# Kernel optimization log

Hardware: AMD Instinct MI355X
Metric: run time of the kernel (lower is better)

The kernel has to match this reference:

```python
import jax, jax.numpy as jnp
import numpy as np

N_NODES = 100000
N_EDGES = 1600000
NUM_FEATURES = 128
NUM_CLASSES = 10
NUM_GRAPHS = 64


def setup_inputs() -> dict:
    key = jax.random.key(0)
    ks = jax.random.split(key, 16)
    x = jax.random.normal(ks[0], (N_NODES, NUM_FEATURES), dtype=jnp.float32)
    edge_index = jax.random.randint(ks[1], (2, N_EDGES), 0, N_NODES, dtype=jnp.int64)
    batch = jnp.sort(jax.random.randint(ks[2], (N_NODES,), 0, NUM_GRAPHS, dtype=jnp.int64))

    def glorot(k, fan_in, fan_out):
        s = jnp.sqrt(6.0 / (fan_in + fan_out)).astype(jnp.float32)
        return jax.random.uniform(k, (fan_in, fan_out), jnp.float32, -s, s)

    dims = [(NUM_FEATURES, 128), (128, 128), (128, 128), (128, 64), (64, 32)]
    params = {}
    for i, (fi, fo) in enumerate(dims, start=1):
        params[f"W{i}"] = glorot(ks[2 + i], fi, fo)
        params[f"b{i}"] = jnp.zeros((fo,), jnp.float32)
    params["Wfc"] = glorot(ks[10], 32, NUM_CLASSES)
    params["bfc"] = jnp.zeros((NUM_CLASSES,), jnp.float32)
    return {"x": x, "edge_index": edge_index, "batch": batch, **params}


def reference(x, edge_index, batch, W1, b1, W2, b2, W3, b3, W4, b4, W5, b5, Wfc, bfc):
    N = x.shape[0]
    loops = jnp.arange(N, dtype=edge_index.dtype)
    src = jnp.concatenate([edge_index[0], loops])  # message source j
    dst = jnp.concatenate([edge_index[1], loops])  # message target i
    # GCN symmetric normalization: deg computed on targets incl. self loops
    deg = jax.ops.segment_sum(jnp.ones_like(dst, x.dtype), dst, num_segments=N)
    dinv = jnp.where(deg > 0, jax.lax.rsqrt(deg), 0.0)
    norm = (dinv[src] * dinv[dst])[:, None]  # [E+N, 1]

    def gcn_conv(h, W, b):
        h = h @ W  # transform first (smaller gather width when out < in)
        msg = h[src] * norm
        return jax.ops.segment_sum(msg, dst, num_segments=N) + b

    h = jax.nn.relu(gcn_conv(x, W1, b1))
    h = jax.nn.relu(gcn_conv(h, W2, b2))
    h = jax.nn.relu(gcn_conv(h, W3, b3))
    h = jax.nn.relu(gcn_conv(h, W4, b4))
    h = jax.nn.relu(gcn_conv(h, W5, b5))

    # global_mean_pool over graph membership
    sums = jax.ops.segment_sum(h, batch, num_segments=NUM_GRAPHS)
    cnts = jax.ops.segment_sum(jnp.ones((N,), h.dtype), batch, num_segments=NUM_GRAPHS)
    pooled = sums / jnp.maximum(cnts, 1.0)[:, None]

    # dropout is identity in eval mode
    return pooled @ Wfc + bfc
```

## Files before the change

kernel.cpp:

```cpp
#include <hip/hip_runtime.h>
#include <hip/hip_bf16.h>

#define N_NODES 100000
#define N_EDGES 1600000
#define N_GRAPHS 64
#define WNB 192
#define BCAP 64

typedef __attribute__((ext_vector_type(8))) short bf16x8;
typedef __attribute__((ext_vector_type(4))) float f32x4;

__device__ inline float bflo(unsigned u) { return __uint_as_float(u << 16); }
__device__ inline float bfhi(unsigned u) { return __uint_as_float(u & 0xffff0000u); }
__device__ inline unsigned short f2bf(float f) {
    unsigned u = __float_as_uint(f);
    return (unsigned short)((u + 0x7fff + ((u >> 16) & 1)) >> 16);
}


__global__ __launch_bounds__(256) void k_setup(int* __restrict__ cursor, int n,
                                               const float* __restrict__ W1,
                                               const float* __restrict__ W2,
                                               const float* __restrict__ W3,
                                               const float* __restrict__ W4,
                                               const float* __restrict__ W5,
                                               unsigned short* __restrict__ wt1,
                                               unsigned short* __restrict__ wt2,
                                               unsigned short* __restrict__ wt3,
                                               unsigned short* __restrict__ wt4,
                                               unsigned short* __restrict__ wt5) {
    const int nb = (N_NODES + 255) / 256;
    if ((int)blockIdx.x < nb) {
        int i = blockIdx.x * 256 + threadIdx.x;
        if (i < n) cursor[i] = i * BCAP;
        return;
    }
    int i = (blockIdx.x - nb) * 256 + threadIdx.x;
    const float* W; unsigned short* WT; int FI, FO, j;
    if (i < 16384)      { W = W1; WT = wt1; FI = 128; FO = 128; j = i; }
    else if (i < 32768) { W = W2; WT = wt2; FI = 128; FO = 128; j = i - 16384; }
    else if (i < 49152) { W = W3; WT = wt3; FI = 128; FO = 128; j = i - 32768; }
    else if (i < 57344) { W = W4; WT = wt4; FI = 128; FO = 64;  j = i - 49152; }
    else if (i < 59392) { W = W5; WT = wt5; FI = 64;  FO = 32;  j = i - 57344; }
    else return;
    int n_ = j / FI, k_ = j % FI;
    WT[j] = f2bf(W[(size_t)k_ * FO + n_]);
}


__global__ __launch_bounds__(256) void k_fillw(const int* __restrict__ ei,
                                               int* __restrict__ cursor,
                                               int* __restrict__ cols, int e) {
    const int w = blockIdx.x & 7;
    const int b = blockIdx.x >> 3;
    const int lo = w * 12500, hi = lo + 12500;
    const int4* d4 = (const int4*)(ei + e);
    const int n4 = e >> 2;
    for (int i = b * 256 + threadIdx.x; i < n4; i += WNB * 256) {
        int4 d = d4[i];
        int base = 4 * i;
        if (d.x >= lo && d.x < hi) {
            int p = atomicAdd(&cursor[d.x], 1);
            if (p < d.x * BCAP + BCAP) cols[p] = ei[base];
        }
        if (d.y >= lo && d.y < hi) {
            int p = atomicAdd(&cursor[d.y], 1);
            if (p < d.y * BCAP + BCAP) cols[p] = ei[base + 1];
        }
        if (d.z >= lo && d.z < hi) {
            int p = atomicAdd(&cursor[d.z], 1);
            if (p < d.z * BCAP + BCAP) cols[p] = ei[base + 2];
        }
        if (d.w >= lo && d.w < hi) {
            int p = atomicAdd(&cursor[d.w], 1);
            if (p < d.w * BCAP + BCAP) cols[p] = ei[base + 3];
        }
    }
}


template <int FI, int FO>
__global__ __launch_bounds__(256) void k_gemm1(const float* __restrict__ Ain,
                                               const unsigned short* __restrict__ WT,
                                               unsigned short* __restrict__ Tout,
                                               const int* __restrict__ cursor,
                                               float* __restrict__ dinv, int n) {
    {
        int gi = blockIdx.x * 256 + threadIdx.x;
        if (gi < n) dinv[gi] = rsqrtf((float)(cursor[gi] - BCAP * gi + 1));
    }
    constexpr int NT = FO / 16;
    constexpr int NC = FI / 32;
    __shared__ unsigned short tile[4][16][FO];
    const int wave = threadIdx.x >> 6;
    const int lane = threadIdx.x & 63;
    const int m = lane & 15;
    const int q = lane >> 4;
    const int row0 = blockIdx.x * 64 + wave * 16;
    int arow = row0 + m;
    if (arow > n - 1) arow = n - 1;

    f32x4 acc[NT];
    #pragma unroll
    for (int j = 0; j < NT; j++) acc[j] = (f32x4){0.f, 0.f, 0.f, 0.f};

    #pragma unroll
    for (int c = 0; c < NC; c++) {
        const int k0 = c * 32 + q * 8;
        const float* ap = Ain + (size_t)arow * FI + k0;
        float4 f0 = *reinterpret_cast<const float4*>(ap);
        float4 f1 = *reinterpret_cast<const float4*>(ap + 4);
        bf16x8 a;
        a[0] = (short)f2bf(f0.x); a[1] = (short)f2bf(f0.y);
        a[2] = (short)f2bf(f0.z); a[3] = (short)f2bf(f0.w);
        a[4] = (short)f2bf(f1.x); a[5] = (short)f2bf(f1.y);
        a[6] = (short)f2bf(f1.z); a[7] = (short)f2bf(f1.w);
        #pragma unroll
        for (int j = 0; j < NT; j++) {
            bf16x8 b = *reinterpret_cast<const bf16x8*>(
                           WT + (size_t)(j * 16 + m) * FI + k0);
            acc[j] = __builtin_amdgcn_mfma_f32_16x16x32_bf16(a, b, acc[j], 0, 0, 0);
        }
    }

    #pragma unroll
    for (int r = 0; r < 4; r++)
        #pragma unroll
        for (int j = 0; j < NT; j++)
            tile[wave][q * 4 + r][j * 16 + m] = f2bf(acc[j][r]);

    constexpr int CPR = FO / 8;
    constexpr int ITERS = 16 * CPR / 64;
    #pragma unroll
    for (int it = 0; it < ITERS; it++) {
        int idx = it * 64 + lane;
        int rr = idx / CPR;
        int cc = idx % CPR;
        int row = row0 + rr;
        if (row < n) {
            uint4 v = *reinterpret_cast<const uint4*>(&tile[wave][rr][cc * 8]);
            *reinterpret_cast<uint4*>(&Tout[(size_t)row * FO + cc * 8]) = v;
        }
    }
}


template <int FA, int FB, int UNR>
__global__ __launch_bounds__(256) void k_fused(const unsigned short* __restrict__ T,
                                               const int* __restrict__ cursor,
                                               const int* __restrict__ cols,
                                               const float* __restrict__ dinv,
                                               const float* __restrict__ bias,
                                               const unsigned short* __restrict__ WT,
                                               unsigned short* __restrict__ Tout, int n) {
    constexpr int LPE = FA / 8;
    constexpr int EPW = 64 / LPE;
    constexpr int STR = FA + 8;
    __shared__ unsigned short hrow[16][STR];

    const int w = threadIdx.x >> 6;
    const int lane = threadIdx.x & 63;
    const int sub = lane / LPE;
    const int li  = lane % LPE;
    const int node0 = blockIdx.x * 16;

    for (int i = 0; i < 4; i++) {
        const int r = w * 4 + i;
        int node = node0 + r;
        bool valid = node < n;
        if (node > n - 1) node = n - 1;
        node = __builtin_amdgcn_readfirstlane(node);

        const float dn = dinv[node];
        float acc[8];
        #pragma unroll
        for (int k = 0; k < 8; k++) acc[k] = 0.f;

        if (sub == 0) {
            float dii = dn * dn;
            uint4 u = reinterpret_cast<const uint4*>(T + (size_t)node * FA)[li];
            acc[0] = dii * bflo(u.x); acc[1] = dii * bfhi(u.x);
            acc[2] = dii * bflo(u.y); acc[3] = dii * bfhi(u.y);
            acc[4] = dii * bflo(u.z); acc[5] = dii * bfhi(u.z);
            acc[6] = dii * bflo(u.w); acc[7] = dii * bfhi(u.w);
        }

        const int e0 = node * BCAP;
        int e1 = cursor[node];
        if (e1 > e0 + BCAP) e1 = e0 + BCAP;
        int e = e0 + sub;
        for (; e + (UNR - 1) * EPW < e1; e += UNR * EPW) {
            int cs[UNR]; float ws[UNR]; uint4 tv[UNR];
            #pragma unroll
            for (int u = 0; u < UNR; u++)
                cs[u] = __builtin_nontemporal_load(&cols[e + u * EPW]);
            #pragma unroll
            for (int u = 0; u < UNR; u++)
                tv[u] = reinterpret_cast<const uint4*>(T + (size_t)cs[u] * FA)[li];
            #pragma unroll
            for (int u = 0; u < UNR; u++)
                ws[u] = dinv[cs[u]] * dn;
            #pragma unroll
            for (int u = 0; u < UNR; u++) {
                float wv = ws[u];
                acc[0] += wv * bflo(tv[u].x); acc[1] += wv * bfhi(tv[u].x);
                acc[2] += wv * bflo(tv[u].y); acc[3] += wv * bfhi(tv[u].y);
                acc[4] += wv * bflo(tv[u].z); acc[5] += wv * bfhi(tv[u].z);
                acc[6] += wv * bflo(tv[u].w); acc[7] += wv * bfhi(tv[u].w);
            }
        }
        for (; e < e1; e += EPW) {
            int c = __builtin_nontemporal_load(&cols[e]);
            uint4 tv = reinterpret_cast<const uint4*>(T + (size_t)c * FA)[li];
            float wv = dinv[c] * dn;
            acc[0] += wv * bflo(tv.x); acc[1] += wv * bfhi(tv.x);
            acc[2] += wv * bflo(tv.y); acc[3] += wv * bfhi(tv.y);
            acc[4] += wv * bflo(tv.z); acc[5] += wv * bfhi(tv.z);
            acc[6] += wv * bflo(tv.w); acc[7] += wv * bfhi(tv.w);
        }

        #pragma unroll
        for (int off = LPE; off < 64; off <<= 1) {
            #pragma unroll
            for (int k = 0; k < 8; k++) acc[k] += __shfl_xor(acc[k], off);
        }

        if (sub == 0) {
            uint4 pk = {0u, 0u, 0u, 0u};
            if (valid) {
                float4 ba = reinterpret_cast<const float4*>(bias)[2 * li];
                float4 bb = reinterpret_cast<const float4*>(bias)[2 * li + 1];
                float r0 = fmaxf(acc[0] + ba.x, 0.f);
                float r1 = fmaxf(acc[1] + ba.y, 0.f);
                float r2 = fmaxf(acc[2] + ba.z, 0.f);
                float r3 = fmaxf(acc[3] + ba.w, 0.f);
                float r4 = fmaxf(acc[4] + bb.x, 0.f);
                float r5 = fmaxf(acc[5] + bb.y, 0.f);
                float r6 = fmaxf(acc[6] + bb.z, 0.f);
                float r7 = fmaxf(acc[7] + bb.w, 0.f);
                pk.x = (unsigned)f2bf(r0) | ((unsigned)f2bf(r1) << 16);
                pk.y = (unsigned)f2bf(r2) | ((unsigned)f2bf(r3) << 16);
                pk.z = (unsigned)f2bf(r4) | ((unsigned)f2bf(r5) << 16);
                pk.w = (unsigned)f2bf(r6) | ((unsigned)f2bf(r7) << 16);
            }
            *reinterpret_cast<uint4*>(&hrow[r][li * 8]) = pk;
        }
    }

    __syncthreads();

    constexpr int NTILES = FB / 16;
    constexpr int NC = FA / 32;
    const int m = lane & 15;
    const int q = lane >> 4;

    for (int j = w; j < NTILES; j += 4) {
        f32x4 acc = (f32x4){0.f, 0.f, 0.f, 0.f};
        #pragma unroll
        for (int c = 0; c < NC; c++) {
            const int k0 = c * 32 + q * 8;
            bf16x8 a = *reinterpret_cast<const bf16x8*>(&hrow[m][k0]);
            bf16x8 b = *reinterpret_cast<const bf16x8*>(
                           WT + (size_t)(j * 16 + m) * FA + k0);
            acc = __builtin_amdgcn_mfma_f32_16x16x32_bf16(a, b, acc, 0, 0, 0);
        }
        #pragma unroll
        for (int r = 0; r < 4; r++) {
            int row = node0 + q * 4 + r;
            if (row < n)
                Tout[(size_t)row * FB + j * 16 + m] = f2bf(acc[r]);
        }
    }
}


template <int FO, int UNR>
__global__ __launch_bounds__(256) void k_agg(const unsigned short* __restrict__ T,
                                             const int* __restrict__ cursor,
                                             const int* __restrict__ cols,
                                             const float* __restrict__ dinv,
                                             const float* __restrict__ bias,
                                             unsigned short* __restrict__ Hout, int n) {
    constexpr int LPE = FO / 8;
    constexpr int EPW = 64 / LPE;
    int node = blockIdx.x * 4 + (threadIdx.x >> 6);
    if (node >= n) return;
    node = __builtin_amdgcn_readfirstlane(node);
    const int lane = threadIdx.x & 63;
    const int sub = lane / LPE;
    const int li  = lane % LPE;

    const float dn = dinv[node];

    float acc[8];
    #pragma unroll
    for (int k = 0; k < 8; k++) acc[k] = 0.f;

    if (sub == 0) {
        float dii = dn * dn;
        uint4 u = reinterpret_cast<const uint4*>(T + (size_t)node * FO)[li];
        acc[0] = dii * bflo(u.x); acc[1] = dii * bfhi(u.x);
        acc[2] = dii * bflo(u.y); acc[3] = dii * bfhi(u.y);
        acc[4] = dii * bflo(u.z); acc[5] = dii * bfhi(u.z);
        acc[6] = dii * bflo(u.w); acc[7] = dii * bfhi(u.w);
    }

    const int e0 = node * BCAP;
    int e1 = cursor[node];
    if (e1 > e0 + BCAP) e1 = e0 + BCAP;
    int e = e0 + sub;
    for (; e + (UNR - 1) * EPW < e1; e += UNR * EPW) {
        int cs[UNR]; float ws[UNR]; uint4 tv[UNR];
        #pragma unroll
        for (int u = 0; u < UNR; u++)
            cs[u] = __builtin_nontemporal_load(&cols[e + u * EPW]);
        #pragma unroll
        for (int u = 0; u < UNR; u++)
            tv[u] = reinterpret_cast<const uint4*>(T + (size_t)cs[u] * FO)[li];
        #pragma unroll
        for (int u = 0; u < UNR; u++)
            ws[u] = dinv[cs[u]] * dn;
        #pragma unroll
        for (int u = 0; u < UNR; u++) {
            float wv = ws[u];
            acc[0] += wv * bflo(tv[u].x); acc[1] += wv * bfhi(tv[u].x);
            acc[2] += wv * bflo(tv[u].y); acc[3] += wv * bfhi(tv[u].y);
            acc[4] += wv * bflo(tv[u].z); acc[5] += wv * bfhi(tv[u].z);
            acc[6] += wv * bflo(tv[u].w); acc[7] += wv * bfhi(tv[u].w);
        }
    }
    for (; e < e1; e += EPW) {
        int c = __builtin_nontemporal_load(&cols[e]);
        uint4 tv = reinterpret_cast<const uint4*>(T + (size_t)c * FO)[li];
        float wv = dinv[c] * dn;
        acc[0] += wv * bflo(tv.x); acc[1] += wv * bfhi(tv.x);
        acc[2] += wv * bflo(tv.y); acc[3] += wv * bfhi(tv.y);
        acc[4] += wv * bflo(tv.z); acc[5] += wv * bfhi(tv.z);
        acc[6] += wv * bflo(tv.w); acc[7] += wv * bfhi(tv.w);
    }

    #pragma unroll
    for (int off = LPE; off < 64; off <<= 1) {
        #pragma unroll
        for (int k = 0; k < 8; k++) acc[k] += __shfl_xor(acc[k], off);
    }

    if (sub == 0) {
        float4 ba = reinterpret_cast<const float4*>(bias)[2 * li];
        float4 bb = reinterpret_cast<const float4*>(bias)[2 * li + 1];
        float r0 = fmaxf(acc[0] + ba.x, 0.f);
        float r1 = fmaxf(acc[1] + ba.y, 0.f);
        float r2 = fmaxf(acc[2] + ba.z, 0.f);
        float r3 = fmaxf(acc[3] + ba.w, 0.f);
        float r4 = fmaxf(acc[4] + bb.x, 0.f);
        float r5 = fmaxf(acc[5] + bb.y, 0.f);
        float r6 = fmaxf(acc[6] + bb.z, 0.f);
        float r7 = fmaxf(acc[7] + bb.w, 0.f);
        uint4 pk;
        pk.x = (unsigned)f2bf(r0) | ((unsigned)f2bf(r1) << 16);
        pk.y = (unsigned)f2bf(r2) | ((unsigned)f2bf(r3) << 16);
        pk.z = (unsigned)f2bf(r4) | ((unsigned)f2bf(r5) << 16);
        pk.w = (unsigned)f2bf(r6) | ((unsigned)f2bf(r7) << 16);
        reinterpret_cast<uint4*>(Hout + (size_t)node * FO)[li] = pk;
    }
}


__global__ __launch_bounds__(256) void k_poolfc(const unsigned short* __restrict__ H,
                                                const int* __restrict__ batch,
                                                const float* __restrict__ Wfc,
                                                const float* __restrict__ bfc,
                                                float* __restrict__ out, int n) {
    __shared__ float red0[256], red1[256];
    __shared__ float pl[32];
    __shared__ int se[2];
    int g = blockIdx.x;
    int t = threadIdx.x;
    if (t < 2) {
        int target = g + t;
        int lo = 0, hi = n;
        while (lo < hi) {
            int mid = (lo + hi) >> 1;
            if (batch[mid] < target) lo = mid + 1; else hi = mid;
        }
        se[t] = lo;
    }
    __syncthreads();
    int s = se[0], e = se[1];
    int c = t & 15;
    int grp = t >> 4;
    float a0 = 0.f, a1 = 0.f;
    for (int i = s + grp; i < e; i += 16) {
        unsigned u = reinterpret_cast<const unsigned*>(H + (size_t)i * 32)[c];
        a0 += bflo(u); a1 += bfhi(u);
    }
    red0[t] = a0; red1[t] = a1;
    __syncthreads();
    for (int off = 128; off >= 16; off >>= 1) {
        if (t < off) { red0[t] += red0[t + off]; red1[t] += red1[t + off]; }
        __syncthreads();
    }
    if (t < 16) {
        float cnt = fmaxf((float)(e - s), 1.0f);
        pl[2 * t]     = red0[t] / cnt;
        pl[2 * t + 1] = red1[t] / cnt;
    }
    __syncthreads();
    if (t < 10) {
        float a = bfc[t];
        #pragma unroll
        for (int k = 0; k < 32; k++) a += pl[k] * Wfc[k * 10 + t];
        out[g * 10 + t] = a;
    }
}


extern "C" void kernel_launch(void* const* d_in, const int* in_sizes, int n_in,
                              void* d_out, int out_size, void* d_ws, size_t ws_size,
                              hipStream_t stream) {
    const int N = N_NODES, E = N_EDGES;

    const float* x     = (const float*)d_in[0];
    const int*   ei    = (const int*)d_in[1];
    const int*   batch = (const int*)d_in[2];
    const float* W1 = (const float*)d_in[3];  const float* b1 = (const float*)d_in[4];
    const float* W2 = (const float*)d_in[5];  const float* b2 = (const float*)d_in[6];
    const float* W3 = (const float*)d_in[7];  const float* b3 = (const float*)d_in[8];
    const float* W4 = (const float*)d_in[9];  const float* b4 = (const float*)d_in[10];
    const float* W5 = (const float*)d_in[11]; const float* b5 = (const float*)d_in[12];
    const float* Wfc = (const float*)d_in[13]; const float* bfc = (const float*)d_in[14];
    float* out = (float*)d_out;

    char* p = (char*)d_ws;
    auto take = [&](size_t b) { char* q = p; p += (b + 511) & ~(size_t)511; return q; };
    int*   cursor = (int*)take((size_t)N * 4);
    float* dinv   = (float*)take((size_t)N * 4);
    int*   cols   = (int*)take((size_t)N * BCAP * 4);
    unsigned short* wt1 = (unsigned short*)take(128 * 128 * 2);
    unsigned short* wt2 = (unsigned short*)take(128 * 128 * 2);
    unsigned short* wt3 = (unsigned short*)take(128 * 128 * 2);
    unsigned short* wt4 = (unsigned short*)take(128 * 64 * 2);
    unsigned short* wt5 = (unsigned short*)take(64 * 32 * 2);
    unsigned short* Ta  = (unsigned short*)take((size_t)N * 128 * 2);
    unsigned short* Tb  = (unsigned short*)take((size_t)N * 128 * 2);

    const int nb = (N + 255) / 256;
    const int gemmb = (N + 63) / 64;
    const int fusedb = (N + 15) / 16;
    const int aggb  = (N + 3) / 4;

    k_setup<<<nb + 232, 256, 0, stream>>>(cursor, N, W1, W2, W3, W4, W5,
                                          wt1, wt2, wt3, wt4, wt5);
    k_fillw<<<8 * WNB, 256, 0, stream>>>(ei, cursor, cols, E);

    k_gemm1<128, 128><<<gemmb, 256, 0, stream>>>(x, wt1, Ta, cursor, dinv, N);
    k_fused<128, 128, 4><<<fusedb, 256, 0, stream>>>(Ta, cursor, cols, dinv, b1, wt2, Tb, N);
    k_fused<128, 128, 4><<<fusedb, 256, 0, stream>>>(Tb, cursor, cols, dinv, b2, wt3, Ta, N);
    k_fused<128, 64, 4><<<fusedb, 256, 0, stream>>>(Ta, cursor, cols, dinv, b3, wt4, Tb, N);
    k_fused<64, 32, 2><<<fusedb, 256, 0, stream>>>(Tb, cursor, cols, dinv, b4, wt5, Ta, N);
    k_agg<32, 1><<<aggb, 256, 0, stream>>>(Ta, cursor, cols, dinv, b5, Tb, N);

    k_poolfc<<<N_GRAPHS, 256, 0, stream>>>(Tb, batch, Wfc, bfc, out, N);
}
```

Measured before the change: 631.9 us.

## Prescale rows by dinv and gather with 16 lanes per node

The symmetric normalization is factored out: each transformed row is pre-multiplied by its own dinv when written (in gemm1 and in the fused epilogue), so the aggregation becomes a plain sum scaled once by the target's dinv. This removes the per-edge dinv[src] gather and multiply. The gather is also restructured so each node gets 16 lanes holding a full row with vector widths matched to the feature size, with int4 column-index prefetching instead of the previous split-edge layout and cross-lane shuffle reduction. Rounding changes slightly because scaling now happens before bf16 storage, and per-node work is serialized over 16 lanes, which may hurt high-degree nodes.

```diff
diff --git a/kernel.cpp b/kernel.cpp
--- a/kernel.cpp
+++ b/kernel.cpp
@@ -79,24 +79,91 @@
 }
 
 
+template <int FA> struct rowvec {};
+template <> struct rowvec<128> { using V = uint4; };
+template <> struct rowvec<64>  { using V = uint2; };
+template <> struct rowvec<32>  { using V = unsigned; };
+
+__device__ inline void upacc(uint4 u, float* a) {
+    a[0] += bflo(u.x); a[1] += bfhi(u.x); a[2] += bflo(u.y); a[3] += bfhi(u.y);
+    a[4] += bflo(u.z); a[5] += bfhi(u.z); a[6] += bflo(u.w); a[7] += bfhi(u.w);
+}
+__device__ inline void upacc(uint2 u, float* a) {
+    a[0] += bflo(u.x); a[1] += bfhi(u.x); a[2] += bflo(u.y); a[3] += bfhi(u.y);
+}
+__device__ inline void upacc(unsigned u, float* a) {
+    a[0] += bflo(u); a[1] += bfhi(u);
+}
+
+template <int FA>
+__device__ inline void gather(const unsigned short* __restrict__ T,
+                              const int* __restrict__ cursor,
+                              const int* __restrict__ cols,
+                              int node, int li, float* acc) {
+    using V = typename rowvec<FA>::V;
+    constexpr int NF = FA / 16;
+    const V* Tp = reinterpret_cast<const V*>(T);
+
+    #pragma unroll
+    for (int k = 0; k < NF; k++) acc[k] = 0.f;
+
+    V us = Tp[(size_t)node * 16 + li];
+    upacc(us, acc);
+
+    const int e0 = node * BCAP;
+    int deg = cursor[node] - e0;
+    if (deg > BCAP) deg = BCAP;
+    const int nch = deg >> 2;
+
+    int4 c0 = {0, 0, 0, 0}, c1 = {0, 0, 0, 0};
+    if (nch > 0) c0 = *reinterpret_cast<const int4*>(cols + e0);
+    if (nch > 1) c1 = *reinterpret_cast<const int4*>(cols + e0 + 4);
+
+    int e = e0;
+    for (int it = 0; it < nch; ++it) {
+        int4 cc = c0;
+        c0 = c1;
+        if (it + 2 < nch) c1 = *reinterpret_cast<const int4*>(cols + e + 8);
+        V t0 = Tp[(size_t)cc.x * 16 + li];
+        V t1 = Tp[(size_t)cc.y * 16 + li];
+        V t2 = Tp[(size_t)cc.z * 16 + li];
+        V t3 = Tp[(size_t)cc.w * 16 + li];
+        upacc(t0, acc); upacc(t1, acc); upacc(t2, acc); upacc(t3, acc);
+        e += 4;
+    }
+    for (int r = e0 + (nch << 2), rend = e0 + deg; r < rend; ++r) {
+        int c = __builtin_nontemporal_load(cols + r);
+        V t = Tp[(size_t)c * 16 + li];
+        upacc(t, acc);
+    }
+}
+
+
 template <int FI, int FO>
 __global__ __launch_bounds__(256) void k_gemm1(const float* __restrict__ Ain,
                                                const unsigned short* __restrict__ WT,
                                                unsigned short* __restrict__ Tout,
                                                const int* __restrict__ cursor,
                                                float* __restrict__ dinv, int n) {
-    {
-        int gi = blockIdx.x * 256 + threadIdx.x;
-        if (gi < n) dinv[gi] = rsqrtf((float)(cursor[gi] - BCAP * gi + 1));
-    }
     constexpr int NT = FO / 16;
     constexpr int NC = FI / 32;
     __shared__ unsigned short tile[4][16][FO];
+    __shared__ float sdv[64];
+    const int row0b = blockIdx.x * 64;
+    if (threadIdx.x < 64) {
+        int r = row0b + threadIdx.x;
+        int rc = r < n ? r : n - 1;
+        float v = rsqrtf((float)(cursor[rc] - BCAP * rc + 1));
+        sdv[threadIdx.x] = v;
+        if (r < n) dinv[r] = v;
+    }
+    __syncthreads();
+
     const int wave = threadIdx.x >> 6;
     const int lane = threadIdx.x & 63;
     const int m = lane & 15;
     const int q = lane >> 4;
-    const int row0 = blockIdx.x * 64 + wave * 16;
+    const int row0 = row0b + wave * 16;
     int arow = row0 + m;
     if (arow > n - 1) arow = n - 1;
 
@@ -124,10 +191,12 @@
     }
 
     #pragma unroll
-    for (int r = 0; r < 4; r++)
+    for (int r = 0; r < 4; r++) {
+        const float dv = sdv[wave * 16 + q * 4 + r];
         #pragma unroll
         for (int j = 0; j < NT; j++)
-            tile[wave][q * 4 + r][j * 16 + m] = f2bf(acc[j][r]);
+            tile[wave][q * 4 + r][j * 16 + m] = f2bf(acc[j][r] * dv);
+    }
 
     constexpr int CPR = FO / 8;
     constexpr int ITERS = 16 * CPR / 64;
@@ -145,7 +214,7 @@
 }
 
 
-template <int FA, int FB, int UNR>
+template <int FA, int FB>
 __global__ __launch_bounds__(256) void k_fused(const unsigned short* __restrict__ T,
                                                const int* __restrict__ cursor,
                                                const int* __restrict__ cols,
@@ -153,98 +222,55 @@
                                                const float* __restrict__ bias,
                                                const unsigned short* __restrict__ WT,
                                                unsigned short* __restrict__ Tout, int n) {
-    constexpr int LPE = FA / 8;
-    constexpr int EPW = 64 / LPE;
+    constexpr int NF = FA / 16;
     constexpr int STR = FA + 8;
     __shared__ unsigned short hrow[16][STR];
+    __shared__ float sdv[16];
 
     const int w = threadIdx.x >> 6;
     const int lane = threadIdx.x & 63;
-    const int sub = lane / LPE;
-    const int li  = lane % LPE;
+    const int sub = lane >> 4;
+    const int li  = lane & 15;
     const int node0 = blockIdx.x * 16;
-
-    for (int i = 0; i < 4; i++) {
-        const int r = w * 4 + i;
-        int node = node0 + r;
-        bool valid = node < n;
-        if (node > n - 1) node = n - 1;
-        node = __builtin_amdgcn_readfirstlane(node);
-
-        const float dn = dinv[node];
-        float acc[8];
-        #pragma unroll
-        for (int k = 0; k < 8; k++) acc[k] = 0.f;
-
-        if (sub == 0) {
-            float dii = dn * dn;
-            uint4 u = reinterpret_cast<const uint4*>(T + (size_t)node * FA)[li];
-            acc[0] = dii * bflo(u.x); acc[1] = dii * bfhi(u.x);
-            acc[2] = dii * bflo(u.y); acc[3] = dii * bfhi(u.y);
-            acc[4] = dii * bflo(u.z); acc[5] = dii * bfhi(u.z);
-            acc[6] = dii * bflo(u.w); acc[7] = dii * bfhi(u.w);
-        }
-
-        const int e0 = node * BCAP;
-        int e1 = cursor[node];
-        if (e1 > e0 + BCAP) e1 = e0 + BCAP;
-        int e = e0 + sub;
-        for (; e + (UNR - 1) * EPW < e1; e += UNR * EPW) {
-            int cs[UNR]; float ws[UNR]; uint4 tv[UNR];
-            #pragma unroll
-            for (int u = 0; u < UNR; u++)
-                cs[u] = __builtin_nontemporal_load(&cols[e + u * EPW]);
-            #pragma unroll
-            for (int u = 0; u < UNR; u++)
-                tv[u] = reinterpret_cast<const uint4*>(T + (size_t)cs[u] * FA)[li];
-            #pragma unroll
-            for (int u = 0; u < UNR; u++)
-                ws[u] = dinv[cs[u]] * dn;
-            #pragma unroll
-            for (int u = 0; u < UNR; u++) {
-                float wv = ws[u];
-                acc[0] += wv * bflo(tv[u].x); acc[1] += wv * bfhi(tv[u].x);
-                acc[2] += wv * bflo(tv[u].y); acc[3] += wv * bfhi(tv[u].y);
-                acc[4] += wv * bflo(tv[u].z); acc[5] += wv * bfhi(tv[u].z);
-                acc[6] += wv * bflo(tv[u].w); acc[7] += wv * bfhi(tv[u].w);
-            }
-        }
-        for (; e < e1; e += EPW) {
-            int c = __builtin_nontemporal_load(&cols[e]);
-            uint4 tv = reinterpret_cast<const uint4*>(T + (size_t)c * FA)[li];
-            float wv = dinv[c] * dn;
-            acc[0] += wv * bflo(tv.x); acc[1] += wv * bfhi(tv.x);
-            acc[2] += wv * bflo(tv.y); acc[3] += wv * bfhi(tv.y);
-            acc[4] += wv * bflo(tv.z); acc[5] += wv * bfhi(tv.z);
-            acc[6] += wv * bflo(tv.w); acc[7] += wv * bfhi(tv.w);
-        }
-
-        #pragma unroll
-        for (int off = LPE; off < 64; off <<= 1) {
-            #pragma unroll
-            for (int k = 0; k < 8; k++) acc[k] += __shfl_xor(acc[k], off);
-        }
-
-        if (sub == 0) {
-            uint4 pk = {0u, 0u, 0u, 0u};
-            if (valid) {
-                float4 ba = reinterpret_cast<const float4*>(bias)[2 * li];
-                float4 bb = reinterpret_cast<const float4*>(bias)[2 * li + 1];
-                float r0 = fmaxf(acc[0] + ba.x, 0.f);
-                float r1 = fmaxf(acc[1] + ba.y, 0.f);
-                float r2 = fmaxf(acc[2] + ba.z, 0.f);
-                float r3 = fmaxf(acc[3] + ba.w, 0.f);
-                float r4 = fmaxf(acc[4] + bb.x, 0.f);
-                float r5 = fmaxf(acc[5] + bb.y, 0.f);
-                float r6 = fmaxf(acc[6] + bb.z, 0.f);
-                float r7 = fmaxf(acc[7] + bb.w, 0.f);
-                pk.x = (unsigned)f2bf(r0) | ((unsigned)f2bf(r1) << 16);
-                pk.y = (unsigned)f2bf(r2) | ((unsigned)f2bf(r3) << 16);
-                pk.z = (unsigned)f2bf(r4) | ((unsigned)f2bf(r5) << 16);
-                pk.w = (unsigned)f2bf(r6) | ((unsigned)f2bf(r7) << 16);
-            }
-            *reinterpret_cast<uint4*>(&hrow[r][li * 8]) = pk;
-        }
+    const int r = w * 4 + sub;
+
+    int node = node0 + r;
+    const bool valid = node < n;
+    if (!valid) node = n - 1;
+
+    const float dn = dinv[node];
+    float acc[NF];
+    gather<FA>(T, cursor, cols, node, li, acc);
+
+    {
+        float b[NF];
+        if constexpr (NF == 8) {
+            float4 ba = reinterpret_cast<const float4*>(bias)[2 * li];
+            float4 bb = reinterpret_cast<const float4*>(bias)[2 * li + 1];
+            b[0] = ba.x; b[1] = ba.y; b[2] = ba.z; b[3] = ba.w;
+            b[4] = bb.x; b[5] = bb.y; b[6] = bb.z; b[7] = bb.w;
+        } else if constexpr (NF == 4) {
+            float4 ba = reinterpret_cast<const float4*>(bias)[li];
+            b[0] = ba.x; b[1] = ba.y; b[2] = ba.z; b[3] = ba.w;
+        } else {
+            float2 ba = reinterpret_cast<const float2*>(bias)[li];
+            b[0] = ba.x; b[1] = ba.y;
+        }
+        unsigned pk[NF / 2];
+        #pragma unroll
+        for (int k = 0; k < NF / 2; k++) {
+            float r0 = fmaxf(fmaf(dn, acc[2 * k], b[2 * k]), 0.f);
+            float r1 = fmaxf(fmaf(dn, acc[2 * k + 1], b[2 * k + 1]), 0.f);
+            pk[k] = (unsigned)f2bf(r0) | ((unsigned)f2bf(r1) << 16);
+        }
+        if constexpr (NF == 8)
+            *reinterpret_cast<uint4*>(&hrow[r][li * 8]) =
+                make_uint4(pk[0], pk[1], pk[2], pk[3]);
+        else if constexpr (NF == 4)
+            *reinterpret_cast<uint2*>(&hrow[r][li * 4]) = make_uint2(pk[0], pk[1]);
+        else
+            *reinterpret_cast<unsigned*>(&hrow[r][li * 2]) = pk[0];
+        if (li == 0) sdv[r] = dn;
     }
 
     __syncthreads();
@@ -255,113 +281,51 @@
     const int q = lane >> 4;
 
     for (int j = w; j < NTILES; j += 4) {
-        f32x4 acc = (f32x4){0.f, 0.f, 0.f, 0.f};
+        f32x4 a4 = (f32x4){0.f, 0.f, 0.f, 0.f};
         #pragma unroll
         for (int c = 0; c < NC; c++) {
             const int k0 = c * 32 + q * 8;
             bf16x8 a = *reinterpret_cast<const bf16x8*>(&hrow[m][k0]);
             bf16x8 b = *reinterpret_cast<const bf16x8*>(
                            WT + (size_t)(j * 16 + m) * FA + k0);
-            acc = __builtin_amdgcn_mfma_f32_16x16x32_bf16(a, b, acc, 0, 0, 0);
-        }
-        #pragma unroll
-        for (int r = 0; r < 4; r++) {
-            int row = node0 + q * 4 + r;
+            a4 = __builtin_amdgcn_mfma_f32_16x16x32_bf16(a, b, a4, 0, 0, 0);
+        }
+        #pragma unroll
+        for (int rr = 0; rr < 4; rr++) {
+            int row = node0 + q * 4 + rr;
             if (row < n)
-                Tout[(size_t)row * FB + j * 16 + m] = f2bf(acc[r]);
-        }
-    }
-}
-
-
-template <int FO, int UNR>
+                Tout[(size_t)row * FB + j * 16 + m] = f2bf(a4[rr] * sdv[q * 4 + rr]);
+        }
+    }
+}
+
+
+template <int FA>
 __global__ __launch_bounds__(256) void k_agg(const unsigned short* __restrict__ T,
                                              const int* __restrict__ cursor,
                                              const int* __restrict__ cols,
                                              const float* __restrict__ dinv,
                                              const float* __restrict__ bias,
                                              unsigned short* __restrict__ Hout, int n) {
-    constexpr int LPE = FO / 8;
-    constexpr int EPW = 64 / LPE;
-    int node = blockIdx.x * 4 + (threadIdx.x >> 6);
-    if (node >= n) return;
-    node = __builtin_amdgcn_readfirstlane(node);
+    const int w = threadIdx.x >> 6;
     const int lane = threadIdx.x & 63;
-    const int sub = lane / LPE;
-    const int li  = lane % LPE;
+    const int sub = lane >> 4;
+    const int li  = lane & 15;
+
+    int node = blockIdx.x * 16 + w * 4 + sub;
+    const bool valid = node < n;
+    if (!valid) node = n - 1;
 
     const float dn = dinv[node];
-
-    float acc[8];
-    #pragma unroll
-    for (int k = 0; k < 8; k++) acc[k] = 0.f;
-
-    if (sub == 0) {
-        float dii = dn * dn;
-        uint4 u = reinterpret_cast<const uint4*>(T + (size_t)node * FO)[li];
-        acc[0] = dii * bflo(u.x); acc[1] = dii * bfhi(u.x);
-        acc[2] = dii * bflo(u.y); acc[3] = dii * bfhi(u.y);
-        acc[4] = dii * bflo(u.z); acc[5] = dii * bfhi(u.z);
-        acc[6] = dii * bflo(u.w); acc[7] = dii * bfhi(u.w);
-    }
-
-    const int e0 = node * BCAP;
-    int e1 = cursor[node];
-    if (e1 > e0 + BCAP) e1 = e0 + BCAP;
-    int e = e0 + sub;
-    for (; e + (UNR - 1) * EPW < e1; e += UNR * EPW) {
-        int cs[UNR]; float ws[UNR]; uint4 tv[UNR];
-        #pragma unroll
-        for (int u = 0; u < UNR; u++)
-            cs[u] = __builtin_nontemporal_load(&cols[e + u * EPW]);
-        #pragma unroll
-        for (int u = 0; u < UNR; u++)
-            tv[u] = reinterpret_cast<const uint4*>(T + (size_t)cs[u] * FO)[li];
-        #pragma unroll
-        for (int u = 0; u < UNR; u++)
-            ws[u] = dinv[cs[u]] * dn;
-        #pragma unroll
-        for (int u = 0; u < UNR; u++) {
-            float wv = ws[u];
-            acc[0] += wv * bflo(tv[u].x); acc[1] += wv * bfhi(tv[u].x);
-            acc[2] += wv * bflo(tv[u].y); acc[3] += wv * bfhi(tv[u].y);
-            acc[4] += wv * bflo(tv[u].z); acc[5] += wv * bfhi(tv[u].z);
-            acc[6] += wv * bflo(tv[u].w); acc[7] += wv * bfhi(tv[u].w);
-        }
-    }
-    for (; e < e1; e += EPW) {
-        int c = __builtin_nontemporal_load(&cols[e]);
-        uint4 tv = reinterpret_cast<const uint4*>(T + (size_t)c * FO)[li];
-        float wv = dinv[c] * dn;
-        acc[0] += wv * bflo(tv.x); acc[1] += wv * bfhi(tv.x);
-        acc[2] += wv * bflo(tv.y); acc[3] += wv * bfhi(tv.y);
-        acc[4] += wv * bflo(tv.z); acc[5] += wv * bfhi(tv.z);
-        acc[6] += wv * bflo(tv.w); acc[7] += wv * bfhi(tv.w);
-    }
-
-    #pragma unroll
-    for (int off = LPE; off < 64; off <<= 1) {
-        #pragma unroll
-        for (int k = 0; k < 8; k++) acc[k] += __shfl_xor(acc[k], off);
-    }
-
-    if (sub == 0) {
-        float4 ba = reinterpret_cast<const float4*>(bias)[2 * li];
-        float4 bb = reinterpret_cast<const float4*>(bias)[2 * li + 1];
-        float r0 = fmaxf(acc[0] + ba.x, 0.f);
-        float r1 = fmaxf(acc[1] + ba.y, 0.f);
-        float r2 = fmaxf(acc[2] + ba.z, 0.f);
-        float r3 = fmaxf(acc[3] + ba.w, 0.f);
-        float r4 = fmaxf(acc[4] + bb.x, 0.f);
-        float r5 = fmaxf(acc[5] + bb.y, 0.f);
-        float r6 = fmaxf(acc[6] + bb.z, 0.f);
-        float r7 = fmaxf(acc[7] + bb.w, 0.f);
-        uint4 pk;
-        pk.x = (unsigned)f2bf(r0) | ((unsigned)f2bf(r1) << 16);
-        pk.y = (unsigned)f2bf(r2) | ((unsigned)f2bf(r3) << 16);
-        pk.z = (unsigned)f2bf(r4) | ((unsigned)f2bf(r5) << 16);
-        pk.w = (unsigned)f2bf(r6) | ((unsigned)f2bf(r7) << 16);
-        reinterpret_cast<uint4*>(Hout + (size_t)node * FO)[li] = pk;
+    float acc[FA / 16];
+    gather<FA>(T, cursor, cols, node, li, acc);
+
+    if (valid) {
+        float2 b2 = reinterpret_cast<const float2*>(bias)[li];
+        float r0 = fmaxf(fmaf(dn, acc[0], b2.x), 0.f);
+        float r1 = fmaxf(fmaf(dn, acc[1], b2.y), 0.f);
+        unsigned pk = (unsigned)f2bf(r0) | ((unsigned)f2bf(r1) << 16);
+        reinterpret_cast<unsigned*>(Hout + (size_t)node * FA)[li] = pk;
     }
 }
 
@@ -447,18 +411,17 @@
     const int nb = (N + 255) / 256;
     const int gemmb = (N + 63) / 64;
     const int fusedb = (N + 15) / 16;
-    const int aggb  = (N + 3) / 4;
 
     k_setup<<<nb + 232, 256, 0, stream>>>(cursor, N, W1, W2, W3, W4, W5,
                                           wt1, wt2, wt3, wt4, wt5);
     k_fillw<<<8 * WNB, 256, 0, stream>>>(ei, cursor, cols, E);
 
     k_gemm1<128, 128><<<gemmb, 256, 0, stream>>>(x, wt1, Ta, cursor, dinv, N);
-    k_fused<128, 128, 4><<<fusedb, 256, 0, stream>>>(Ta, cursor, cols, dinv, b1, wt2, Tb, N);
-    k_fused<128, 128, 4><<<fusedb, 256, 0, stream>>>(Tb, cursor, cols, dinv, b2, wt3, Ta, N);
-    k_fused<128, 64, 4><<<fusedb, 256, 0, stream>>>(Ta, cursor, cols, dinv, b3, wt4, Tb, N);
-    k_fused<64, 32, 2><<<fusedb, 256, 0, stream>>>(Tb, cursor, cols, dinv, b4, wt5, Ta, N);
-    k_agg<32, 1><<<aggb, 256, 0, stream>>>(Ta, cursor, cols, dinv, b5, Tb, N);
+    k_fused<128, 128><<<fusedb, 256, 0, stream>>>(Ta, cursor, cols, dinv, b1, wt2, Tb, N);
+    k_fused<128, 128><<<fusedb, 256, 0, stream>>>(Tb, cursor, cols, dinv, b2, wt3, Ta, N);
+    k_fused<128, 64><<<fusedb, 256, 0, stream>>>(Ta, cursor, cols, dinv, b3, wt4, Tb, N);
+    k_fused<64, 32><<<fusedb, 256, 0, stream>>>(Tb, cursor, cols, dinv, b4, wt5, Ta, N);
+    k_agg<32><<<fusedb, 256, 0, stream>>>(Ta, cursor, cols, dinv, b5, Tb, N);
 
     k_poolfc<<<N_GRAPHS, 256, 0, stream>>>(Tb, batch, Wfc, bfc, out, N);
 }
```

Result: faster. 538.9 us (-14.7%).
